# Performance work log

Hardware: AMD Instinct MI355X
Metric: run time of the kernel (lower is better)

The kernel has to match this reference:

```python
import jax, jax.numpy as jnp
import numpy as np

B = 65536      # batch
N_IN = 784     # n_input_neurons
D = 10         # n_neurons_per_hidd_bank
NB = 10        # banks per layer (layer0 = input banks 0-9, layer1 = output banks 10-19)
N_OUT = 10     # n_output_neurons
N_HIDD_BANKS = 20


def setup_inputs() -> dict:
    key = jax.random.key(0)
    ks = jax.random.split(key, 10)
    s_in = 1.0 / np.sqrt(N_IN)
    s_d = 1.0 / np.sqrt(D)
    return {
        "x": jax.random.normal(ks[0], (B, N_IN), dtype=jnp.float32),
        # input-bank linears: 784 -> 10, one per input bank
        "W_in": jax.random.uniform(ks[1], (NB, N_IN, D), jnp.float32, -s_in, s_in),
        "b_in": jax.random.uniform(ks[2], (NB, D), jnp.float32, -s_in, s_in),
        # gate linears per (source, target) connection: 10 -> 1
        "W_gate": jax.random.uniform(ks[3], (NB, NB, D), jnp.float32, -s_d, s_d),
        "b_gate": jax.random.uniform(ks[4], (NB, NB), jnp.float32, -s_d, s_d),
        # data linears per (source, target) connection: 10 -> 10
        "W_data": jax.random.uniform(ks[5], (NB, NB, D, D), jnp.float32, -s_d, s_d),
        "b_data": jax.random.uniform(ks[6], (NB, NB, D), jnp.float32, -s_d, s_d),
        # output-bank linears: 10 -> 10, one per output bank
        "W_out": jax.random.uniform(ks[7], (NB, D, N_OUT), jnp.float32, -s_d, s_d),
        "b_out": jax.random.uniform(ks[8], (NB, N_OUT), jnp.float32, -s_d, s_d),
    }


def reference(x, W_in, b_in, W_gate, b_gate, W_data, b_data, W_out, b_out):
    # Input banks (banks 0-9): relu(Linear_784->10)
    acts0 = jax.nn.relu(jnp.einsum("bi,sid->sbd", x, W_in) + b_in[:, None, :])  # [S,B,D]

    # Gates: original checks gate_act.data[0,0] > 0, i.e. scalar from batch row 0 only.
    gate = jnp.einsum("sd,std->st", acts0[:, 0, :], W_gate) + b_gate  # [S,T]
    mask = (gate > 0.0).astype(x.dtype)                               # [S,T] binary, detached

    # Per-connection data linears (bias included per open connection, as in original)
    data = jnp.einsum("sbd,stde->stbe", acts0, W_data) + b_data[:, :, None, :]  # [S,T,B,D]
    target_pre = jnp.einsum("st,stbe->tbe", mask, data)                          # [T,B,D]
    acts1 = jax.nn.relu(target_pre)                                              # [T,B,D]

    # A target bank is active (non-None) iff any incoming gate is open; its output
    # linear (including bias) only contributes when active.
    any_open = (jnp.sum(mask, axis=0) > 0.0).astype(x.dtype)  # [T]
    out_contrib = jnp.einsum("tbe,teo->tbo", acts1, W_out) + b_out[:, None, :]
    logits = jnp.einsum("t,tbo->bo", any_open, out_contrib)   # [B,N_OUT]

    output = jax.nn.log_softmax(logits, axis=1)
    prob_open_gate = jnp.sum(mask) / N_HIDD_BANKS
    return output, prob_open_gate
```

## Files before the change

kernel.cpp:

```cpp
#include <hip/hip_runtime.h>
#include <math.h>

#define BATCH   65536
#define N_IN    784
#define DD      10
#define NB      10
#define SD      100
#define N_OUTS  10
#define TILES   16
#define ROWST   16
#define XSTRIDE 1616
#define XBUFB   (16 * XSTRIDE)

typedef float  f32x4  __attribute__((ext_vector_type(4)));
typedef short  bf16x8 __attribute__((ext_vector_type(8)));

#define WTF_F 0
#define WDF_F 51200
#define WOF_F 59392
#define BD_F  60416
#define WO_F  60544
#define BL_F  61664
#define MK_F  61680

__device__ __forceinline__ short f2bf(float f) {
    unsigned u = __builtin_bit_cast(unsigned, f);
    unsigned r = u + 0x7fffu + ((u >> 16) & 1u);
    return (short)(r >> 16);
}

#define BAR_LGKM() do {                                          \
    asm volatile("s_waitcnt lgkmcnt(0)" ::: "memory");           \
    __builtin_amdgcn_s_barrier();                                \
    __builtin_amdgcn_sched_barrier(0); } while (0)

__global__ __launch_bounds__(1024) void prep1_kernel(
                             const float* __restrict__ x,
                             const float* __restrict__ W_in,
                             const float* __restrict__ b_in,
                             const float* __restrict__ W_gate,
                             const float* __restrict__ b_gate,
                             const float* __restrict__ b_data,
                             const float* __restrict__ W_out,
                             const float* __restrict__ b_out,
                             float* __restrict__ out,
                             float* __restrict__ ws) {
    __shared__ float a0r0[SD];
    __shared__ float mask_l[SD];
    __shared__ float ao_l[NB];
    const int tid = threadIdx.x;

    if (tid < 800) {
        int c = tid >> 3, h = tid & 7;
        int s = c / DD, d = c % DD;
        const float* wcol = W_in + s * (N_IN * DD) + d;
        float acc = 0.f;
        int i0 = h * 98;
        #pragma unroll 14
        for (int i = i0; i < i0 + 98; ++i)
            acc += x[i] * wcol[i * DD];
        acc += __shfl_xor(acc, 1, 64);
        acc += __shfl_xor(acc, 2, 64);
        acc += __shfl_xor(acc, 4, 64);
        if (h == 0) a0r0[c] = fmaxf(acc + b_in[c], 0.f);
    }
    __syncthreads();

    if (tid < SD) {
        float g = b_gate[tid];
        int s = tid / DD;
        for (int d = 0; d < DD; ++d)
            g += a0r0[s * DD + d] * W_gate[tid * DD + d];
        mask_l[tid] = (g > 0.f) ? 1.f : 0.f;
    }
    __syncthreads();

    if (tid < NB) {
        float any = 0.f;
        for (int s = 0; s < NB; ++s) any = fmaxf(any, mask_l[s * DD + tid]);
        ao_l[tid] = any;
    }
    if (tid == 0) {
        float sum = 0.f;
        for (int i = 0; i < SD; ++i) sum += mask_l[i];
        out[(long)BATCH * N_OUTS] = sum / 20.0f;
    }
    __syncthreads();

    if (tid < SD) ws[MK_F + tid] = mask_l[tid];

    for (int idx = tid; idx < 128; idx += blockDim.x) {
        float v = 0.f;
        if (idx < SD) {
            int t = idx / DD, e = idx % DD;
            for (int s = 0; s < NB; ++s)
                v += mask_l[s * DD + t] * b_data[(s * NB + t) * DD + e];
        }
        ws[BD_F + idx] = v;
    }
    for (int idx = tid; idx < 10 * 112; idx += blockDim.x) {
        int o = idx / 112, te = idx % 112;
        float v = 0.f;
        if (te < SD) {
            int t = te / DD, e = te % DD;
            v = ao_l[t] * W_out[(t * DD + e) * N_OUTS + o];
        }
        ws[WO_F + idx] = v;
    }
    if (tid < N_OUTS) {
        float v = 0.f;
        for (int t = 0; t < NB; ++t) v += ao_l[t] * b_out[t * N_OUTS + tid];
        ws[BL_F + tid] = v;
    }
}

__global__ void prep2_kernel(const float* __restrict__ W_in,
                             const float* __restrict__ W_data,
                             float* __restrict__ ws) {
    short* wtf = (short*)(ws + WTF_F);
    short* wdf = (short*)(ws + WDF_F);
    short* wof = (short*)(ws + WOF_F);
    const float* mask = ws + MK_F;
    const int n1 = 25 * 8 * 512;
    const int n2 = 4 * 8 * 512;
    const int n3 = 4 * 512;
    for (int idx = blockIdx.x * blockDim.x + threadIdx.x; idx < n1 + n2 + n3;
         idx += gridDim.x * blockDim.x) {
        if (idx < n1) {
            int K = idx / 4096, rem = idx % 4096;
            int ct = rem / 512, l2 = rem % 512;
            int l = l2 >> 3, e = l2 & 7;
            int r = l & 15, g = l >> 4;
            int c = 16 * ct + r, k = K * 32 + g * 8 + e;
            float v = (c < SD && k < N_IN)
                          ? W_in[(c / DD) * (N_IN * DD) + k * DD + (c % DD)] : 0.f;
            wtf[idx] = f2bf(v);
        } else if (idx < n1 + n2) {
            int i2 = idx - n1;
            int kk = i2 / 4096, rem = i2 % 4096;
            int ct = rem / 512, l2 = rem % 512;
            int l = l2 >> 3, e = l2 & 7;
            int r = l & 15, g = l >> 4;
            int m = 16 * ct + r, k = kk * 32 + g * 8 + e;
            float v = 0.f;
            if (m < SD && k < SD) {
                int t = m / DD, eo = m % DD, s = k / DD, d = k % DD;
                v = mask[s * DD + t] * W_data[((s * NB + t) * DD + d) * DD + eo];
            }
            wdf[i2] = f2bf(v);
        } else {
            int i3 = idx - n1 - n2;
            int kk = i3 / 512, l2 = i3 % 512;
            int l = l2 >> 3, e = l2 & 7;
            int o = l & 15, g = l >> 4;
            int te = kk * 32 + g * 8 + e;
            float v = (o < 10 && te < 112) ? ws[WO_F + o * 112 + te] : 0.f;
            wof[i3] = f2bf(v);
        }
    }
}

__global__ __launch_bounds__(512, 1) void main_kernel(
        const float* __restrict__ x,
        const float* __restrict__ b_in,
        const float* __restrict__ ws,
        float* __restrict__ out) {
    __shared__ __align__(16) unsigned char xb16[2][XBUFB];
    __shared__ __align__(16) short a0b[16 * 136];
    __shared__ __align__(16) short a1b[16 * 136];

    const int tid  = threadIdx.x;
    const int w    = tid >> 6;
    const int lane = tid & 63;
    const int g    = lane >> 4;
    const int r    = lane & 15;
    const size_t rowbase = (size_t)blockIdx.x * (TILES * ROWST);
    const float4* xblk = (const float4*)(x + rowbase * N_IN);

    const short* wtf = (const short*)(ws + WTF_F);
    const short* wdf = (const short*)(ws + WDF_F);
    const short* wof = (const short*)(ws + WOF_F);

    int loff[7];
    #pragma unroll
    for (int q = 0; q < 7; ++q) {
        int idx = tid + 512 * q;
        int row = idx / 196, col = idx - row * 196;
        if (row > 15) row = 15;
        loff[q] = row * XSTRIDE + col * 8;
    }

    bf16x8 wt[25];
    #pragma unroll
    for (int K = 0; K < 25; ++K)
        wt[K] = *(const bf16x8*)(wtf + (K * 8 + w) * 512 + lane * 8);
    bf16x8 wd[4], wo[4];
    #pragma unroll
    for (int kk = 0; kk < 4; ++kk) {
        wd[kk] = *(const bf16x8*)(wdf + (kk * 8 + w) * 512 + lane * 8);
        wo[kk] = *(const bf16x8*)(wof + kk * 512 + lane * 8);
    }
    float bi[4], bd[4], blv[4];
    #pragma unroll
    for (int j = 0; j < 4; ++j) {
        int c = 16 * w + 4 * g + j;
        bi[j] = (c < SD) ? b_in[c] : 0.f;
        bd[j] = ws[BD_F + c];
        int o = 4 * g + j;
        blv[j] = (o < 10) ? ws[BL_F + o] : 0.f;
    }

    float4 xr[7];

#define STAGE_LOAD(t) do {                                                     \
    const float4* _s = xblk + (size_t)(t) * 3136;                              \
    _Pragma("unroll")                                                          \
    for (int _q = 0; _q < 6; ++_q)                                             \
        xr[_q] = _s[tid + 512 * _q];                                           \
    if (tid < 64) xr[6] = _s[tid + 3072];                                      \
    __builtin_amdgcn_sched_barrier(0);                                         \
} while (0)

#define STAGE_WRITE(bufp) do {                                                 \
    _Pragma("unroll")                                                          \
    for (int _q = 0; _q < 6; ++_q) {                                           \
        unsigned _u0, _u1;                                                     \
        asm("v_cvt_pk_bf16_f32 %0, %1, %2"                                     \
            : "=v"(_u0) : "v"(xr[_q].x), "v"(xr[_q].y));                       \
        asm("v_cvt_pk_bf16_f32 %0, %1, %2"                                     \
            : "=v"(_u1) : "v"(xr[_q].z), "v"(xr[_q].w));                       \
        *(uint2*)((bufp) + loff[_q]) = make_uint2(_u0, _u1);                   \
    }                                                                          \
    if (tid < 64) {                                                            \
        unsigned _u0, _u1;                                                     \
        asm("v_cvt_pk_bf16_f32 %0, %1, %2"                                     \
            : "=v"(_u0) : "v"(xr[6].x), "v"(xr[6].y));                         \
        asm("v_cvt_pk_bf16_f32 %0, %1, %2"                                     \
            : "=v"(_u1) : "v"(xr[6].z), "v"(xr[6].w));                         \
        *(uint2*)((bufp) + loff[6]) = make_uint2(_u0, _u1);                    \
    }                                                                          \
} while (0)

    STAGE_LOAD(0);
    for (int i = tid; i < 192; i += 512) {
        int buf = i / 96, rem = i - buf * 96;
        int row = rem / 6, p = rem - row * 6;
        *(uint2*)(&xb16[buf][0] + row * XSTRIDE + 1568 + p * 8) = make_uint2(0u, 0u);
    }
    STAGE_WRITE(&xb16[0][0]);
    BAR_LGKM();

    for (int t = 0; t < TILES; ++t) {
        const int cur = t & 1;
        if (t + 1 < TILES) STAGE_LOAD(t + 1);

        f32x4 acc = (f32x4){0.f, 0.f, 0.f, 0.f};
        const unsigned char* xbr = &xb16[cur][0] + r * XSTRIDE + g * 16;
        #pragma unroll
        for (int K = 0; K < 25; ++K) {
            bf16x8 bf = *(const bf16x8*)(xbr + K * 64);
            acc = __builtin_amdgcn_mfma_f32_16x16x32_bf16(wt[K], bf, acc, 0, 0, 0);
        }
        {
            short* myrow = a0b + r * 136;
            int c0 = 16 * w + 4 * g;
            float v0 = fmaxf(acc[0] + bi[0], 0.f), v1 = fmaxf(acc[1] + bi[1], 0.f);
            float v2 = fmaxf(acc[2] + bi[2], 0.f), v3 = fmaxf(acc[3] + bi[3], 0.f);
            unsigned p01, p23;
            asm("v_cvt_pk_bf16_f32 %0, %1, %2" : "=v"(p01) : "v"(v0), "v"(v1));
            asm("v_cvt_pk_bf16_f32 %0, %1, %2" : "=v"(p23) : "v"(v2), "v"(v3));
            *(uint2*)(myrow + c0) = make_uint2(p01, p23);
        }
        BAR_LGKM();

        f32x4 acc2 = (f32x4){0.f, 0.f, 0.f, 0.f};
        #pragma unroll
        for (int kk = 0; kk < 4; ++kk) {
            bf16x8 bf = *(const bf16x8*)(a0b + r * 136 + kk * 32 + g * 8);
            acc2 = __builtin_amdgcn_mfma_f32_16x16x32_bf16(wd[kk], bf, acc2, 0, 0, 0);
        }
        {
            short* myrow = a1b + r * 136;
            int c0 = 16 * w + 4 * g;
            float v0 = fmaxf(acc2[0] + bd[0], 0.f), v1 = fmaxf(acc2[1] + bd[1], 0.f);
            float v2 = fmaxf(acc2[2] + bd[2], 0.f), v3 = fmaxf(acc2[3] + bd[3], 0.f);
            unsigned p01, p23;
            asm("v_cvt_pk_bf16_f32 %0, %1, %2" : "=v"(p01) : "v"(v0), "v"(v1));
            asm("v_cvt_pk_bf16_f32 %0, %1, %2" : "=v"(p23) : "v"(v2), "v"(v3));
            *(uint2*)(myrow + c0) = make_uint2(p01, p23);
        }
        BAR_LGKM();

        if (t + 1 < TILES) STAGE_WRITE(&xb16[cur ^ 1][0]);

        f32x4 accL = (f32x4){0.f, 0.f, 0.f, 0.f};
        #pragma unroll
        for (int kk = 0; kk < 4; ++kk) {
            bf16x8 bf = *(const bf16x8*)(a1b + r * 136 + kk * 32 + g * 8);
            accL = __builtin_amdgcn_mfma_f32_16x16x32_bf16(wo[kk], bf, accL, 0, 0, 0);
        }
        float lgf[4];
        #pragma unroll
        for (int j = 0; j < 4; ++j)
            lgf[j] = (4 * g + j < 10) ? accL[j] + blv[j] : -1e30f;

        float m = fmaxf(fmaxf(lgf[0], lgf[1]), fmaxf(lgf[2], lgf[3]));
        m = fmaxf(m, __shfl_xor(m, 16, 64));
        m = fmaxf(m, __shfl_xor(m, 32, 64));
        float s = expf(lgf[0] - m) + expf(lgf[1] - m)
                + expf(lgf[2] - m) + expf(lgf[3] - m);
        s += __shfl_xor(s, 16, 64);
        s += __shfl_xor(s, 32, 64);
        float z = m + logf(s);

        if ((r >> 1) == w) {
            float* ob = out + (rowbase + (size_t)t * ROWST + r) * N_OUTS + 4 * g;
            if (g < 3) *(float2*)(ob)     = make_float2(lgf[0] - z, lgf[1] - z);
            if (g < 2) *(float2*)(ob + 2) = make_float2(lgf[2] - z, lgf[3] - z);
        }
        BAR_LGKM();
    }
#undef STAGE_LOAD
#undef STAGE_WRITE
}

extern "C" void kernel_launch(void* const* d_in, const int* in_sizes, int n_in,
                              void* d_out, int out_size, void* d_ws, size_t ws_size,
                              hipStream_t stream) {
    const float* x      = (const float*)d_in[0];
    const float* W_in   = (const float*)d_in[1];
    const float* b_in   = (const float*)d_in[2];
    const float* W_gate = (const float*)d_in[3];
    const float* b_gate = (const float*)d_in[4];
    const float* W_data = (const float*)d_in[5];
    const float* b_data = (const float*)d_in[6];
    const float* W_out  = (const float*)d_in[7];
    const float* b_out  = (const float*)d_in[8];
    float* out = (float*)d_out;
    float* ws  = (float*)d_ws;

    prep1_kernel<<<1, 1024, 0, stream>>>(x, W_in, b_in, W_gate, b_gate,
                                         b_data, W_out, b_out, out, ws);
    prep2_kernel<<<256, 256, 0, stream>>>(W_in, W_data, ws);
    main_kernel<<<256, 512, 0, stream>>>(x, b_in, ws, out);
}
```

Before: 67.14 us.

## Merge prep kernels and double-buffer activation tiles to drop a barrier

Folds the two weight-prep kernels into one launch. Block 0 computes the gate mask and writes the mask-dependent data and output weights directly. The other 256 blocks repack W_in in parallel, removing a kernel launch and a dependency round trip through the workspace. In the main loop, the a0/a1 activation buffers are double-buffered by tile parity, which lets the trailing per-tile barrier be removed and the x stage write be moved before the second barrier. This costs extra LDS and relies on the parity buffers being correctly ordered across iterations.

After: 68.17 us. About the same (+1.5%).

```diff
diff --git a/kernel.cpp b/kernel.cpp
--- a/kernel.cpp
+++ b/kernel.cpp
@@ -19,9 +19,7 @@
 #define WDF_F 51200
 #define WOF_F 59392
 #define BD_F  60416
-#define WO_F  60544
-#define BL_F  61664
-#define MK_F  61680
+#define BL_F  60544
 
 __device__ __forceinline__ short f2bf(float f) {
     unsigned u = __builtin_bit_cast(unsigned, f);
@@ -34,21 +32,39 @@
     __builtin_amdgcn_s_barrier();                                \
     __builtin_amdgcn_sched_barrier(0); } while (0)
 
-__global__ __launch_bounds__(1024) void prep1_kernel(
+__global__ __launch_bounds__(1024) void prep_kernel(
                              const float* __restrict__ x,
                              const float* __restrict__ W_in,
                              const float* __restrict__ b_in,
                              const float* __restrict__ W_gate,
                              const float* __restrict__ b_gate,
+                             const float* __restrict__ W_data,
                              const float* __restrict__ b_data,
                              const float* __restrict__ W_out,
                              const float* __restrict__ b_out,
                              float* __restrict__ out,
                              float* __restrict__ ws) {
+    const int tid = threadIdx.x;
+
+    if (blockIdx.x != 0) {
+        short* wtf = (short*)(ws + WTF_F);
+        int idx = (int)(blockIdx.x - 1) * 1024 + tid;
+        if (idx < 25 * 8 * 512) {
+            int K = idx / 4096, rem = idx % 4096;
+            int ct = rem / 512, l2 = rem % 512;
+            int l = l2 >> 3, e = l2 & 7;
+            int r = l & 15, g = l >> 4;
+            int c = 16 * ct + r, k = K * 32 + g * 8 + e;
+            float v = (c < SD && k < N_IN)
+                          ? W_in[(c / DD) * (N_IN * DD) + k * DD + (c % DD)] : 0.f;
+            wtf[idx] = f2bf(v);
+        }
+        return;
+    }
+
     __shared__ float a0r0[SD];
     __shared__ float mask_l[SD];
     __shared__ float ao_l[NB];
-    const int tid = threadIdx.x;
 
     if (tid < 800) {
         int c = tid >> 3, h = tid & 7;
@@ -87,57 +103,10 @@
     }
     __syncthreads();
 
-    if (tid < SD) ws[MK_F + tid] = mask_l[tid];
-
-    for (int idx = tid; idx < 128; idx += blockDim.x) {
-        float v = 0.f;
-        if (idx < SD) {
-            int t = idx / DD, e = idx % DD;
-            for (int s = 0; s < NB; ++s)
-                v += mask_l[s * DD + t] * b_data[(s * NB + t) * DD + e];
-        }
-        ws[BD_F + idx] = v;
-    }
-    for (int idx = tid; idx < 10 * 112; idx += blockDim.x) {
-        int o = idx / 112, te = idx % 112;
-        float v = 0.f;
-        if (te < SD) {
-            int t = te / DD, e = te % DD;
-            v = ao_l[t] * W_out[(t * DD + e) * N_OUTS + o];
-        }
-        ws[WO_F + idx] = v;
-    }
-    if (tid < N_OUTS) {
-        float v = 0.f;
-        for (int t = 0; t < NB; ++t) v += ao_l[t] * b_out[t * N_OUTS + tid];
-        ws[BL_F + tid] = v;
-    }
-}
-
-__global__ void prep2_kernel(const float* __restrict__ W_in,
-                             const float* __restrict__ W_data,
-                             float* __restrict__ ws) {
-    short* wtf = (short*)(ws + WTF_F);
-    short* wdf = (short*)(ws + WDF_F);
-    short* wof = (short*)(ws + WOF_F);
-    const float* mask = ws + MK_F;
-    const int n1 = 25 * 8 * 512;
-    const int n2 = 4 * 8 * 512;
-    const int n3 = 4 * 512;
-    for (int idx = blockIdx.x * blockDim.x + threadIdx.x; idx < n1 + n2 + n3;
-         idx += gridDim.x * blockDim.x) {
-        if (idx < n1) {
-            int K = idx / 4096, rem = idx % 4096;
-            int ct = rem / 512, l2 = rem % 512;
-            int l = l2 >> 3, e = l2 & 7;
-            int r = l & 15, g = l >> 4;
-            int c = 16 * ct + r, k = K * 32 + g * 8 + e;
-            float v = (c < SD && k < N_IN)
-                          ? W_in[(c / DD) * (N_IN * DD) + k * DD + (c % DD)] : 0.f;
-            wtf[idx] = f2bf(v);
-        } else if (idx < n1 + n2) {
-            int i2 = idx - n1;
-            int kk = i2 / 4096, rem = i2 % 4096;
+    {
+        short* wdf = (short*)(ws + WDF_F);
+        for (int idx = tid; idx < 4 * 8 * 512; idx += 1024) {
+            int kk = idx / 4096, rem = idx % 4096;
             int ct = rem / 512, l2 = rem % 512;
             int l = l2 >> 3, e = l2 & 7;
             int r = l & 15, g = l >> 4;
@@ -145,18 +114,39 @@
             float v = 0.f;
             if (m < SD && k < SD) {
                 int t = m / DD, eo = m % DD, s = k / DD, d = k % DD;
-                v = mask[s * DD + t] * W_data[((s * NB + t) * DD + d) * DD + eo];
-            }
-            wdf[i2] = f2bf(v);
-        } else {
-            int i3 = idx - n1 - n2;
-            int kk = i3 / 512, l2 = i3 % 512;
+                v = mask_l[s * DD + t] * W_data[((s * NB + t) * DD + d) * DD + eo];
+            }
+            wdf[idx] = f2bf(v);
+        }
+    }
+    {
+        short* wof = (short*)(ws + WOF_F);
+        for (int idx = tid; idx < 4 * 512; idx += 1024) {
+            int kk = idx / 512, l2 = idx % 512;
             int l = l2 >> 3, e = l2 & 7;
             int o = l & 15, g = l >> 4;
             int te = kk * 32 + g * 8 + e;
-            float v = (o < 10 && te < 112) ? ws[WO_F + o * 112 + te] : 0.f;
-            wof[i3] = f2bf(v);
-        }
+            float v = 0.f;
+            if (o < 10 && te < SD) {
+                int t = te / DD, eo = te % DD;
+                v = ao_l[t] * W_out[(t * DD + eo) * N_OUTS + o];
+            }
+            wof[idx] = f2bf(v);
+        }
+    }
+    if (tid < 128) {
+        float v = 0.f;
+        if (tid < SD) {
+            int t = tid / DD, e = tid % DD;
+            for (int s = 0; s < NB; ++s)
+                v += mask_l[s * DD + t] * b_data[(s * NB + t) * DD + e];
+        }
+        ws[BD_F + tid] = v;
+    }
+    if (tid < N_OUTS) {
+        float v = 0.f;
+        for (int t = 0; t < NB; ++t) v += ao_l[t] * b_out[t * N_OUTS + tid];
+        ws[BL_F + tid] = v;
     }
 }
 
@@ -166,8 +156,8 @@
         const float* __restrict__ ws,
         float* __restrict__ out) {
     __shared__ __align__(16) unsigned char xb16[2][XBUFB];
-    __shared__ __align__(16) short a0b[16 * 136];
-    __shared__ __align__(16) short a1b[16 * 136];
+    __shared__ __align__(16) short a0b[2][16 * 136];
+    __shared__ __align__(16) short a1b[2][16 * 136];
 
     const int tid  = threadIdx.x;
     const int w    = tid >> 6;
@@ -254,15 +244,15 @@
         const int cur = t & 1;
         if (t + 1 < TILES) STAGE_LOAD(t + 1);
 
-        f32x4 acc = (f32x4){0.f, 0.f, 0.f, 0.f};
-        const unsigned char* xbr = &xb16[cur][0] + r * XSTRIDE + g * 16;
-        #pragma unroll
-        for (int K = 0; K < 25; ++K) {
-            bf16x8 bf = *(const bf16x8*)(xbr + K * 64);
-            acc = __builtin_amdgcn_mfma_f32_16x16x32_bf16(wt[K], bf, acc, 0, 0, 0);
-        }
         {
-            short* myrow = a0b + r * 136;
+            f32x4 acc = (f32x4){0.f, 0.f, 0.f, 0.f};
+            const unsigned char* xbr = &xb16[cur][0] + r * XSTRIDE + g * 16;
+            #pragma unroll
+            for (int K = 0; K < 25; ++K) {
+                bf16x8 bf = *(const bf16x8*)(xbr + K * 64);
+                acc = __builtin_amdgcn_mfma_f32_16x16x32_bf16(wt[K], bf, acc, 0, 0, 0);
+            }
+            short* myrow = &a0b[cur][0] + r * 136;
             int c0 = 16 * w + 4 * g;
             float v0 = fmaxf(acc[0] + bi[0], 0.f), v1 = fmaxf(acc[1] + bi[1], 0.f);
             float v2 = fmaxf(acc[2] + bi[2], 0.f), v3 = fmaxf(acc[3] + bi[3], 0.f);
@@ -273,14 +263,14 @@
         }
         BAR_LGKM();
 
-        f32x4 acc2 = (f32x4){0.f, 0.f, 0.f, 0.f};
-        #pragma unroll
-        for (int kk = 0; kk < 4; ++kk) {
-            bf16x8 bf = *(const bf16x8*)(a0b + r * 136 + kk * 32 + g * 8);
-            acc2 = __builtin_amdgcn_mfma_f32_16x16x32_bf16(wd[kk], bf, acc2, 0, 0, 0);
-        }
         {
-            short* myrow = a1b + r * 136;
+            f32x4 acc2 = (f32x4){0.f, 0.f, 0.f, 0.f};
+            #pragma unroll
+            for (int kk = 0; kk < 4; ++kk) {
+                bf16x8 bf = *(const bf16x8*)(&a0b[cur][0] + r * 136 + kk * 32 + g * 8);
+                acc2 = __builtin_amdgcn_mfma_f32_16x16x32_bf16(wd[kk], bf, acc2, 0, 0, 0);
+            }
+            short* myrow = &a1b[cur][0] + r * 136;
             int c0 = 16 * w + 4 * g;
             float v0 = fmaxf(acc2[0] + bd[0], 0.f), v1 = fmaxf(acc2[1] + bd[1], 0.f);
             float v2 = fmaxf(acc2[2] + bd[2], 0.f), v3 = fmaxf(acc2[3] + bd[3], 0.f);
@@ -289,36 +279,36 @@
             asm("v_cvt_pk_bf16_f32 %0, %1, %2" : "=v"(p23) : "v"(v2), "v"(v3));
             *(uint2*)(myrow + c0) = make_uint2(p01, p23);
         }
+        if (t + 1 < TILES) STAGE_WRITE(&xb16[cur ^ 1][0]);
         BAR_LGKM();
 
-        if (t + 1 < TILES) STAGE_WRITE(&xb16[cur ^ 1][0]);
-
-        f32x4 accL = (f32x4){0.f, 0.f, 0.f, 0.f};
-        #pragma unroll
-        for (int kk = 0; kk < 4; ++kk) {
-            bf16x8 bf = *(const bf16x8*)(a1b + r * 136 + kk * 32 + g * 8);
-            accL = __builtin_amdgcn_mfma_f32_16x16x32_bf16(wo[kk], bf, accL, 0, 0, 0);
-        }
-        float lgf[4];
-        #pragma unroll
-        for (int j = 0; j < 4; ++j)
-            lgf[j] = (4 * g + j < 10) ? accL[j] + blv[j] : -1e30f;
-
-        float m = fmaxf(fmaxf(lgf[0], lgf[1]), fmaxf(lgf[2], lgf[3]));
-        m = fmaxf(m, __shfl_xor(m, 16, 64));
-        m = fmaxf(m, __shfl_xor(m, 32, 64));
-        float s = expf(lgf[0] - m) + expf(lgf[1] - m)
-                + expf(lgf[2] - m) + expf(lgf[3] - m);
-        s += __shfl_xor(s, 16, 64);
-        s += __shfl_xor(s, 32, 64);
-        float z = m + logf(s);
-
-        if ((r >> 1) == w) {
-            float* ob = out + (rowbase + (size_t)t * ROWST + r) * N_OUTS + 4 * g;
-            if (g < 3) *(float2*)(ob)     = make_float2(lgf[0] - z, lgf[1] - z);
-            if (g < 2) *(float2*)(ob + 2) = make_float2(lgf[2] - z, lgf[3] - z);
-        }
-        BAR_LGKM();
+        {
+            f32x4 accL = (f32x4){0.f, 0.f, 0.f, 0.f};
+            #pragma unroll
+            for (int kk = 0; kk < 4; ++kk) {
+                bf16x8 bf = *(const bf16x8*)(&a1b[cur][0] + r * 136 + kk * 32 + g * 8);
+                accL = __builtin_amdgcn_mfma_f32_16x16x32_bf16(wo[kk], bf, accL, 0, 0, 0);
+            }
+            float lgf[4];
+            #pragma unroll
+            for (int j = 0; j < 4; ++j)
+                lgf[j] = (4 * g + j < 10) ? accL[j] + blv[j] : -1e30f;
+
+            float m = fmaxf(fmaxf(lgf[0], lgf[1]), fmaxf(lgf[2], lgf[3]));
+            m = fmaxf(m, __shfl_xor(m, 16, 64));
+            m = fmaxf(m, __shfl_xor(m, 32, 64));
+            float s = expf(lgf[0] - m) + expf(lgf[1] - m)
+                    + expf(lgf[2] - m) + expf(lgf[3] - m);
+            s += __shfl_xor(s, 16, 64);
+            s += __shfl_xor(s, 32, 64);
+            float z = m + logf(s);
+
+            if ((r >> 1) == w) {
+                float* ob = out + (rowbase + (size_t)t * ROWST + r) * N_OUTS + 4 * g;
+                if (g < 3) *(float2*)(ob)     = make_float2(lgf[0] - z, lgf[1] - z);
+                if (g < 2) *(float2*)(ob + 2) = make_float2(lgf[2] - z, lgf[3] - z);
+            }
+        }
     }
 #undef STAGE_LOAD
 #undef STAGE_WRITE
@@ -339,8 +329,7 @@
     float* out = (float*)d_out;
     float* ws  = (float*)d_ws;
 
-    prep1_kernel<<<1, 1024, 0, stream>>>(x, W_in, b_in, W_gate, b_gate,
-                                         b_data, W_out, b_out, out, ws);
-    prep2_kernel<<<256, 256, 0, stream>>>(W_in, W_data, ws);
+    prep_kernel<<<257, 1024, 0, stream>>>(x, W_in, b_in, W_gate, b_gate,
+                                          W_data, b_data, W_out, b_out, out, ws);
     main_kernel<<<256, 512, 0, stream>>>(x, b_in, ws, out);
 }
```
